# Optimization experiments

Measured on AMD Instinct MI355X. Metric: run time of the kernel, lower is better.

## Reference

```python
import jax, jax.numpy as jnp
import numpy as np

N_GROUPS = 32  # getGroupSize(.) assumed -> channels // 8 (or //24 for 3*ch) == 32 for ch=256
HEADS = 4


def group_norm(x, gamma, beta, groups=N_GROUPS, eps=1e-5):
    n, c = x.shape
    xg = x.reshape(n, groups, c // groups)
    mu = xg.mean(-1, keepdims=True)
    var = xg.var(-1, keepdims=True)
    xn = ((xg - mu) * jax.lax.rsqrt(var + eps)).reshape(n, c)
    return xn * gamma + beta


def setup_inputs():
    key = jax.random.key(0)
    N, E, CH, HID = 2000, 16000, 256, 256
    ks = jax.random.split(key, 24)

    def w(k, shape, s=0.02):
        return (jax.random.normal(k, shape) * s).astype(jnp.float32)

    inp = {
        'x': jax.random.normal(ks[0], (N, CH), jnp.float32),
        'edge_index': jax.random.randint(ks[1], (2, E), 0, N),
        'edge_attr': jax.random.normal(ks[2], (E, CH), jnp.float32),
        # edge_mlp: GN(3ch)+ReLU -> Linear(3ch,hid) -> GN(hid)+ReLU -> Linear(hid,ch)
        'gn_e1_g': jnp.ones((3 * CH,), jnp.float32), 'gn_e1_b': jnp.zeros((3 * CH,), jnp.float32),
        'We1': w(ks[3], (3 * CH, HID)), 'be1': jnp.zeros((HID,), jnp.float32),
        'gn_e2_g': jnp.ones((HID,), jnp.float32), 'gn_e2_b': jnp.zeros((HID,), jnp.float32),
        'We2': w(ks[4], (HID, CH)), 'be2': jnp.zeros((CH,), jnp.float32),
        # actN: GN(ch)+ReLU
        'gn_n_g': jnp.ones((CH,), jnp.float32), 'gn_n_b': jnp.zeros((CH,), jnp.float32),
        # multi-head attention projections
        'Wq': w(ks[5], (CH, CH)), 'bq': jnp.zeros((CH,), jnp.float32),
        'Wk': w(ks[6], (CH, CH)), 'bk': jnp.zeros((CH,), jnp.float32),
        'Wv': w(ks[7], (CH, CH)), 'bv': jnp.zeros((CH,), jnp.float32),
        'Wo': w(ks[8], (CH, CH)), 'bo': jnp.zeros((CH,), jnp.float32),
        # node_mlp: Linear(2ch,hid) -> GN(hid)+ReLU -> Linear(hid,ch)
        'Wn1': w(ks[9], (2 * CH, HID)), 'bn1': jnp.zeros((HID,), jnp.float32),
        'gn_n2_g': jnp.ones((HID,), jnp.float32), 'gn_n2_b': jnp.zeros((HID,), jnp.float32),
        'Wn2': w(ks[10], (HID, CH)), 'bn2': jnp.zeros((CH,), jnp.float32),
    }
    return inp


def reference(x, edge_index, edge_attr,
              gn_e1_g, gn_e1_b, We1, be1, gn_e2_g, gn_e2_b, We2, be2,
              gn_n_g, gn_n_b, Wq, bq, Wk, bk, Wv, bv, Wo, bo,
              Wn1, bn1, gn_n2_g, gn_n2_b, Wn2, bn2):
    row, col = edge_index[0], edge_index[1]
    N, ch = x.shape
    E = edge_attr.shape[0]
    dk = ch // HEADS

    # ---- edge model: cat(src, tgt, e) -> GN/ReLU -> Lin -> GN/ReLU -> Lin (+res) ----
    e_in = jnp.concatenate([x[row], x[col], edge_attr], axis=1)  # [E, 3ch]
    h = jax.nn.relu(group_norm(e_in, gn_e1_g, gn_e1_b))
    h = h @ We1 + be1
    h = jax.nn.relu(group_norm(h, gn_e2_g, gn_e2_b))
    e_out = h @ We2 + be2 + edge_attr  # [E, ch]

    # ---- node model: dense-masked MHA, queries=nodes, keys/values=edges ----
    mask = jnp.zeros((N, E), x.dtype).at[col, jnp.arange(E)].set(1.0)  # scatter adjacency
    q = (x @ Wq + bq).reshape(N, HEADS, dk)
    k = (e_out @ Wk + bk).reshape(E, HEADS, dk)
    v = (e_out @ Wv + bv).reshape(E, HEADS, dk)
    scores = jnp.einsum('nhd,ehd->hne', q, k) / jnp.sqrt(jnp.float32(dk))  # [H, N, E]
    scores = jnp.where(mask[None] > 0, scores, jnp.float32(-1e9))
    attn = jax.nn.softmax(scores, axis=-1)
    g = jnp.einsum('hne,ehd->nhd', attn, v).reshape(N, ch) @ Wo + bo  # [N, ch]

    xa = jax.nn.relu(group_norm(x, gn_n_g, gn_n_b))
    h = jnp.concatenate([xa, g], axis=1) @ Wn1 + bn1  # thinker='cat'
    h = jax.nn.relu(group_norm(h, gn_n2_g, gn_n2_b))
    n_out = h @ Wn2 + bn2 + x  # residual

    return n_out, e_out
```

## Files before the change

kernel.cpp:

```cpp
#include <hip/hip_runtime.h>
#include <hip/hip_bf16.h>
#include <stdint.h>
#include <math.h>

#define CH 256

typedef __attribute__((ext_vector_type(8)))  short short8;
typedef __attribute__((ext_vector_type(16))) short short16;
typedef __attribute__((ext_vector_type(4)))  float f32x4;

#define GL2LDS16(g, l) __builtin_amdgcn_global_load_lds(                       \
    (const __attribute__((address_space(1))) void*)(g),                        \
    (__attribute__((address_space(3))) void*)(l), 16, 0, 0)

__device__ inline short f2bf(float f) {
    __hip_bfloat16 h = __float2bfloat16(f);
    short s;
    __builtin_memcpy(&s, &h, 2);
    return s;
}

__device__ inline float bf2f(short s) {
    unsigned u = ((unsigned)(unsigned short)s) << 16;
    float f;
    __builtin_memcpy(&f, &u, 4);
    return f;
}

__device__ inline float warp_sum64(float v) {
    v += __shfl_xor(v, 32, 64);
    v += __shfl_xor(v, 16, 64);
    v += __shfl_xor(v, 8, 64);
    v += __shfl_xor(v, 4, 64);
    v += __shfl_xor(v, 2, 64);
    v += __shfl_xor(v, 1, 64);
    return v;
}

__device__ inline float warp_max64(float v) {
    v = fmaxf(v, __shfl_xor(v, 32, 64));
    v = fmaxf(v, __shfl_xor(v, 16, 64));
    v = fmaxf(v, __shfl_xor(v, 8, 64));
    v = fmaxf(v, __shfl_xor(v, 4, 64));
    v = fmaxf(v, __shfl_xor(v, 2, 64));
    v = fmaxf(v, __shfl_xor(v, 1, 64));
    return v;
}

struct GArgs {
    const short* A; const short* Bt; const float* bias; const float* res;
    float* C; short* Cbf;
    const float* gamma; const float* beta; float* vbar;
    int M, K, Nc, ldc, coff;
    const short* A2; const short* Bt2; const float* bias2; short* Cbf2;
    int M2, Nc2, y_split;
    const int* coli;
    int* cursor; int* elist;
    const int* counts; int* offsets; int Nn;
};

template <int BM, int BN, int EPI, int DUAL, int VB, int FILL,
          int SCAN = 0, int PAN2 = 0, int XSWZ = 0>
__global__ __launch_bounds__(256) void mfma_gemm(GArgs g)
{
    constexpr int BK = 64;
    constexpr int HM = BM / 2, HN = BN / 2;
    constexpr int FM = HM / 16, FN = HN / 16;
    constexpr int PA = BM / 32;
    constexpr int PB = BN / 32;
    constexpr int NP2 = PAN2 ? 2 : 1;
    __shared__ short As[BM * BK];
    __shared__ short Bs[NP2 * BN * BK];

    const short* A = g.A; const short* Bt = g.Bt;
    const float* bias = g.bias; const float* res = g.res;
    float* C = g.C; short* Cbf = g.Cbf;
    int M = g.M, ldc = g.ldc, co = g.coff;
    const int K = g.K;
    int by = blockIdx.y, bx = blockIdx.x;

    if constexpr (SCAN) {
        if (by == (int)gridDim.y - 1) {
            const int t0 = threadIdx.x;
            if (bx == 0) {
                int* ss = (int*)As;
                int base8 = t0 * 8;
                int loc[8]; int srun = 0;
                #pragma unroll
                for (int j = 0; j < 8; j++) {
                    int idx = base8 + j;
                    int c = (idx < g.Nn) ? g.counts[idx] : 0;
                    loc[j] = srun; srun += c;
                }
                ss[t0] = srun;
                __syncthreads();
                for (int off = 1; off < 256; off <<= 1) {
                    int v = (t0 >= off) ? ss[t0 - off] : 0;
                    __syncthreads();
                    ss[t0] += v;
                    __syncthreads();
                }
                int excl = (t0 > 0) ? ss[t0 - 1] : 0;
                #pragma unroll
                for (int j = 0; j < 8; j++) {
                    int idx = base8 + j;
                    if (idx < g.Nn) {
                        int v = excl + loc[j];
                        g.offsets[idx] = v;
                        g.cursor[idx]  = v;
                    }
                }
                if (t0 == 255) g.offsets[g.Nn] = ss[255];
            }
            return;
        }
    }

    bool qrole = false;
    if constexpr (DUAL) {
        if (by >= g.y_split) {
            by -= g.y_split;
            if (bx * BN >= g.Nc2) return;
            qrole = true;
            A = g.A2; Bt = g.Bt2; bias = g.bias2; Cbf = g.Cbf2;
            C = nullptr; res = nullptr;
            M = g.M2; ldc = g.Nc2; co = 0;
        }
    }

    if constexpr (XSWZ) {
        if (!qrole) {
            int h = by * 4 + bx;
            int lby = (h >> 5) * 8 + (h & 7);
            if (lby * BM >= M) return;
            by = lby;
            bx = (h >> 3) & 3;
        }
    }

    const int t = threadIdx.x;
    const int wave = t >> 6, lane = t & 63;
    const int q = lane >> 4, l16 = lane & 15;
    const int row0 = by * BM;
    const int col0 = bx * BN;
    const int wm = wave & 1, wn = wave >> 1;

    if constexpr (FILL) {
        if (!qrole && bx == 0 && t < BM) {
            int rg = row0 + t;
            if (rg < M) {
                int c = g.coli[rg];
                int p = atomicAdd(&g.cursor[c], 1);
                g.elist[p] = rg;
            }
        }
    }

    f32x4 acc[NP2][FM][FN];
    #pragma unroll
    for (int p2 = 0; p2 < NP2; p2++)
        #pragma unroll
        for (int i = 0; i < FM; i++)
            #pragma unroll
            for (int j = 0; j < FN; j++) acc[p2][i][j] = (f32x4){0.f, 0.f, 0.f, 0.f};

    for (int k0 = 0; k0 < K; k0 += BK) {
        #pragma unroll
        for (int p = 0; p < PA; p++) {
            int chunk = p * 256 + t;
            int r = chunk >> 3;
            int cs = (((chunk & 7) ^ (r & 7)) * 8);
            int gr = row0 + r; if (gr >= M) gr = M - 1;
            const short* gsrc = A + (size_t)gr * K + k0 + cs;
            short* ldst = &As[(p * 256 + wave * 64) * 8];
            GL2LDS16(gsrc, ldst);
        }
        #pragma unroll
        for (int p2 = 0; p2 < NP2; p2++) {
            if (!(PAN2 && p2 == 1 && qrole)) {
                #pragma unroll
                for (int p = 0; p < PB; p++) {
                    int chunk = p * 256 + t;
                    int r = chunk >> 3;
                    int cs = (((chunk & 7) ^ (r & 7)) * 8);
                    const short* gsrc = Bt + (size_t)(col0 + p2 * 256 + r) * K + k0 + cs;
                    short* ldst = &Bs[p2 * BN * BK + (p * 256 + wave * 64) * 8];
                    GL2LDS16(gsrc, ldst);
                }
            }
        }
        __syncthreads();
        #pragma unroll
        for (int ks = 0; ks < 2; ks++) {
            short8 af[FM];
            #pragma unroll
            for (int mi = 0; mi < FM; mi++) {
                int R = wm * HM + mi * 16 + l16;
                int slot = ((ks * 4 + q) ^ (R & 7)) * 8;
                af[mi] = *(const short8*)&As[R * BK + slot];
            }
            #pragma unroll
            for (int p2 = 0; p2 < NP2; p2++) {
                if (!(PAN2 && p2 == 1 && qrole)) {
                    short8 bfr[FN];
                    #pragma unroll
                    for (int ni = 0; ni < FN; ni++) {
                        int R = wn * HN + ni * 16 + l16;
                        int slot = ((ks * 4 + q) ^ (R & 7)) * 8;
                        bfr[ni] = *(const short8*)&Bs[p2 * BN * BK + R * BK + slot];
                    }
                    #pragma unroll
                    for (int mi = 0; mi < FM; mi++)
                        #pragma unroll
                        for (int ni = 0; ni < FN; ni++)
                            acc[p2][mi][ni] = __builtin_amdgcn_mfma_f32_16x16x32_bf16(
                                af[mi], bfr[ni], acc[p2][mi][ni], 0, 0, 0);
                }
            }
        }
        __syncthreads();
    }

    #pragma unroll
    for (int p2 = 0; p2 < NP2; p2++) {
        if (PAN2 && p2 == 1 && qrole) continue;
        #pragma unroll
        for (int ni = 0; ni < FN; ni++) {
            int cg = col0 + p2 * 256 + wn * HN + ni * 16 + l16;
            float bv = bias[cg];
            if constexpr (EPI == 1) {
                float ga = g.gamma[cg], be = g.beta[cg];
                #pragma unroll
                for (int mi = 0; mi < FM; mi++) {
                    #pragma unroll
                    for (int r = 0; r < 4; r++) {
                        float v = acc[p2][mi][ni][r] + bv;
                        float s = v, sq = v * v;
                        s += __shfl_xor(s, 1, 64);  sq += __shfl_xor(sq, 1, 64);
                        s += __shfl_xor(s, 2, 64);  sq += __shfl_xor(sq, 2, 64);
                        s += __shfl_xor(s, 4, 64);  sq += __shfl_xor(sq, 4, 64);
                        float mean = s * 0.125f;
                        float var = sq * 0.125f - mean * mean;
                        float o = fmaxf((v - mean) * rsqrtf(var + 1e-5f) * ga + be, 0.f);
                        int rg = row0 + wm * HM + mi * 16 + q * 4 + r;
                        if (rg < M) Cbf[(size_t)rg * ldc + co + cg] = f2bf(o);
                    }
                }
            } else {
                #pragma unroll
                for (int mi = 0; mi < FM; mi++) {
                    #pragma unroll
                    for (int r = 0; r < 4; r++) {
                        int rg = row0 + wm * HM + mi * 16 + q * 4 + r;
                        if (rg < M) {
                            float v = acc[p2][mi][ni][r] + bv;
                            if (res) v += res[(size_t)rg * ldc + co + cg];
                            if (C)   C[(size_t)rg * ldc + co + cg] = v;
                            if (Cbf) Cbf[(size_t)rg * ldc + co + cg] = f2bf(v);
                        }
                    }
                }
                if constexpr (VB) {
                    bool vpanel = PAN2 ? (p2 == 1) : (!qrole && cg >= 256);
                    if (vpanel) {
                        float part = 0.f;
                        #pragma unroll
                        for (int mi = 0; mi < FM; mi++)
                            #pragma unroll
                            for (int r = 0; r < 4; r++) {
                                int rg = row0 + wm * HM + mi * 16 + q * 4 + r;
                                if (rg < M) part += acc[p2][mi][ni][r] + bv;
                            }
                        part += __shfl_xor(part, 16, 64);
                        part += __shfl_xor(part, 32, 64);
                        if (q == 0) atomicAdd(&g.vbar[cg - 256], part);
                    }
                }
            }
        }
    }
}

struct PrepPack {
    const float* wsrc[8];
    short* wdst[8];
    int wK[8];
    int wstart[8];
    int NW, NP;
    const float* x;
    short* x_bf;
    short* cat_bf;
    float2* xs;
    const float* gng;
    const float* gnb;
    float* vbar;
    const float* bk;
    const float* bv;
    float* bkv;
    int* counts;
    int N;
};

__global__ __launch_bounds__(256) void prep_kernel(PrepPack p)
{
    int bid = blockIdx.x;
    int t = threadIdx.x;
    if (bid < p.NW) {
        int m = 0;
        #pragma unroll
        for (int i = 1; i < 8; i++) if (bid >= p.wstart[i]) m = i;
        int k0 = (bid - p.wstart[m]) * 16;
        const float* src = p.wsrc[m];
        short16 o;
        #pragma unroll
        for (int j = 0; j < 16; j++) o[j] = f2bf(src[(size_t)(k0 + j) * 256 + t]);
        *(short16*)(p.wdst[m] + (size_t)t * p.wK[m] + k0) = o;
        return;
    }
    if (bid >= p.NW + p.NP) {
        int i = (bid - p.NW - p.NP) * 256 + t;
        if (i < p.N) p.counts[i] = 0;
        return;
    }
    int pb = bid - p.NW;
    if (pb == 0) {
        p.vbar[t] = 0.f;
        p.bkv[t] = p.bk[t];
        p.bkv[256 + t] = p.bv[t];
    }
    int r = pb * 8 + (t >> 5);
    int g = t & 31;
    if (r >= p.N) return;
    size_t xb = (size_t)r * CH + g * 8;
    float4 a = *(const float4*)&p.x[xb];
    float4 b = *(const float4*)&p.x[xb + 4];
    short8 xr;
    xr[0] = f2bf(a.x); xr[1] = f2bf(a.y); xr[2] = f2bf(a.z); xr[3] = f2bf(a.w);
    xr[4] = f2bf(b.x); xr[5] = f2bf(b.y); xr[6] = f2bf(b.z); xr[7] = f2bf(b.w);
    *(short8*)&p.x_bf[xb] = xr;
    float s  = a.x + a.y + a.z + a.w + b.x + b.y + b.z + b.w;
    float s2 = a.x*a.x + a.y*a.y + a.z*a.z + a.w*a.w
             + b.x*b.x + b.y*b.y + b.z*b.z + b.w*b.w;
    p.xs[(size_t)r * 32 + g] = make_float2(s, s2);
    float m = s * 0.125f;
    float var = s2 * 0.125f - m * m;
    float rsd = rsqrtf(var + 1e-5f);
    float4 g0 = *(const float4*)&p.gng[g * 8];
    float4 g1 = *(const float4*)&p.gng[g * 8 + 4];
    float4 b0 = *(const float4*)&p.gnb[g * 8];
    float4 b1 = *(const float4*)&p.gnb[g * 8 + 4];
    short8 o;
    o[0] = f2bf(fmaxf((a.x - m) * rsd * g0.x + b0.x, 0.f));
    o[1] = f2bf(fmaxf((a.y - m) * rsd * g0.y + b0.y, 0.f));
    o[2] = f2bf(fmaxf((a.z - m) * rsd * g0.z + b0.z, 0.f));
    o[3] = f2bf(fmaxf((a.w - m) * rsd * g0.w + b0.w, 0.f));
    o[4] = f2bf(fmaxf((b.x - m) * rsd * g1.x + b1.x, 0.f));
    o[5] = f2bf(fmaxf((b.y - m) * rsd * g1.y + b1.y, 0.f));
    o[6] = f2bf(fmaxf((b.z - m) * rsd * g1.z + b1.z, 0.f));
    o[7] = f2bf(fmaxf((b.w - m) * rsd * g1.w + b1.w, 0.f));
    *(short8*)&p.cat_bf[(size_t)r * (2 * CH) + g * 8] = o;
}

__global__ __launch_bounds__(256) void estats_kernel(
    const float* __restrict__ eattr, const int* __restrict__ rowi,
    const int* __restrict__ coli, const float2* __restrict__ xs,
    const short* __restrict__ x_bf,
    const float* __restrict__ g1v, const float* __restrict__ b1v,
    short* __restrict__ e1n, int* __restrict__ counts, int E)
{
    __shared__ float2 ea[8][32];
    __shared__ float2 musr[8][32];
    int t = threadIdx.x;
    int slot = t >> 5, g = t & 31;
    int e = blockIdx.x * 8 + slot;
    float4 a = *(const float4*)&eattr[(size_t)e * CH + g * 8];
    float4 b = *(const float4*)&eattr[(size_t)e * CH + g * 8 + 4];
    float s  = a.x + a.y + a.z + a.w + b.x + b.y + b.z + b.w;
    float s2 = a.x*a.x + a.y*a.y + a.z*a.z + a.w*a.w
             + b.x*b.x + b.y*b.y + b.z*b.z + b.w*b.w;
    ea[slot][g] = make_float2(s, s2);
    int r = rowi[e], c = coli[e];
    if (g == 0) atomicAdd(&counts[c], 1);
    __syncthreads();
    float S = 0.f, S2 = 0.f;
    #pragma unroll
    for (int j = 0; j < 3; j++) {
        int b3 = 3 * g + j;
        int src = b3 >> 5, idx = b3 & 31;
        float2 v;
        if (src == 0)      v = xs[(size_t)r * 32 + idx];
        else if (src == 1) v = xs[(size_t)c * 32 + idx];
        else               v = ea[slot][idx];
        S += v.x; S2 += v.y;
    }
    float m = S * (1.f / 24.f);
    float var = S2 * (1.f / 24.f) - m * m;
    musr[slot][g] = make_float2(m, rsqrtf(var + 1e-5f));
    __syncthreads();
    #pragma unroll
    for (int seg = 0; seg < 3; seg++) {
        int pos = seg * 256 + g * 8;
        float2 ms = musr[slot][pos / 24];
        float4 ga  = *(const float4*)&g1v[pos];
        float4 ga2 = *(const float4*)&g1v[pos + 4];
        float4 gb  = *(const float4*)&b1v[pos];
        float4 gb2 = *(const float4*)&b1v[pos + 4];
        float v0, v1, v2, v3, v4, v5, v6, v7;
        if (seg == 2) {
            v0 = a.x; v1 = a.y; v2 = a.z; v3 = a.w;
            v4 = b.x; v5 = b.y; v6 = b.z; v7 = b.w;
        } else {
            const short* srow = x_bf + (size_t)(seg == 0 ? r : c) * CH + g * 8;
            short8 v8 = *(const short8*)srow;
            v0 = bf2f(v8[0]); v1 = bf2f(v8[1]); v2 = bf2f(v8[2]); v3 = bf2f(v8[3]);
            v4 = bf2f(v8[4]); v5 = bf2f(v8[5]); v6 = bf2f(v8[6]); v7 = bf2f(v8[7]);
        }
        short8 o;
        o[0] = f2bf(fmaxf((v0 - ms.x) * ms.y * ga.x  + gb.x,  0.f));
        o[1] = f2bf(fmaxf((v1 - ms.x) * ms.y * ga.y  + gb.y,  0.f));
        o[2] = f2bf(fmaxf((v2 - ms.x) * ms.y * ga.z  + gb.z,  0.f));
        o[3] = f2bf(fmaxf((v3 - ms.x) * ms.y * ga.w  + gb.w,  0.f));
        o[4] = f2bf(fmaxf((v4 - ms.x) * ms.y * ga2.x + gb2.x, 0.f));
        o[5] = f2bf(fmaxf((v5 - ms.x) * ms.y * ga2.y + gb2.y, 0.f));
        o[6] = f2bf(fmaxf((v6 - ms.x) * ms.y * ga2.z + gb2.z, 0.f));
        o[7] = f2bf(fmaxf((v7 - ms.x) * ms.y * ga2.w + gb2.w, 0.f));
        *(short8*)&e1n[(size_t)e * 768 + pos] = o;
    }
}

__global__ __launch_bounds__(256) void attn_kernel(
    const short* __restrict__ qb, const short* __restrict__ kvb,
    const int* __restrict__ offsets, const int* __restrict__ elist,
    const float* __restrict__ vbar, short* __restrict__ g_bf, int N, int E)
{
    __shared__ int eidx[64];
    __shared__ float scl[4 * 64];
    int n = blockIdx.x;
    int wave = threadIdx.x >> 6;
    int lane = threadIdx.x & 63;
    int s0 = offsets[n], s1 = offsets[n + 1];
    float q0 = bf2f(qb[(size_t)n * CH + lane]);
    float q1 = bf2f(qb[(size_t)n * CH + 64 + lane]);
    float q2 = bf2f(qb[(size_t)n * CH + 128 + lane]);
    float q3 = bf2f(qb[(size_t)n * CH + 192 + lane]);
    float out = 0.f, m = -INFINITY, l = 0.f;
    for (int base = s0; base < s1; base += 64) {
        int cn = s1 - base; if (cn > 64) cn = 64;
        if (wave == 0 && lane < cn) eidx[lane] = elist[base + lane];
        __syncthreads();
        for (int j = wave; j < cn; j += 4) {
            int e = eidx[j];
            const short* kr = kvb + (size_t)e * 512;
            float d0 = warp_sum64(q0 * bf2f(kr[lane]));
            float d1 = warp_sum64(q1 * bf2f(kr[64 + lane]));
            float d2 = warp_sum64(q2 * bf2f(kr[128 + lane]));
            float d3 = warp_sum64(q3 * bf2f(kr[192 + lane]));
            if (lane == 0) {
                scl[j]       = d0 * 0.125f;
                scl[64 + j]  = d1 * 0.125f;
                scl[128 + j] = d2 * 0.125f;
                scl[192 + j] = d3 * 0.125f;
            }
        }
        __syncthreads();
        float s = (lane < cn) ? scl[wave * 64 + lane] : -INFINITY;
        float mc = warp_max64(s);
        float nm = fmaxf(m, mc);
        float scale = __expf(m - nm);
        float pp = (lane < cn) ? __expf(s - nm) : 0.f;
        float ps = warp_sum64(pp);
        l = l * scale + ps;
        out *= scale;
        m = nm;
        for (int i = 0; i < cn; i++) {
            float pi = __shfl(pp, i, 64);
            int ei = eidx[i];
            out += pi * bf2f(kvb[(size_t)ei * 512 + 256 + wave * 64 + lane]);
        }
        __syncthreads();
    }
    float res;
    if (s1 > s0) res = out / l;
    else         res = vbar[wave * 64 + lane] * (1.f / (float)E);
    g_bf[(size_t)n * CH + wave * 64 + lane] = f2bf(res);
}

extern "C" void kernel_launch(void* const* d_in, const int* in_sizes, int n_in,
                              void* d_out, int out_size, void* d_ws, size_t ws_size,
                              hipStream_t stream)
{
    const float* x       = (const float*)d_in[0];
    const int*   ei      = (const int*)d_in[1];
    const float* eattr   = (const float*)d_in[2];
    const float* gn_e1_g = (const float*)d_in[3];
    const float* gn_e1_b = (const float*)d_in[4];
    const float* We1     = (const float*)d_in[5];
    const float* be1     = (const float*)d_in[6];
    const float* gn_e2_g = (const float*)d_in[7];
    const float* gn_e2_b = (const float*)d_in[8];
    const float* We2     = (const float*)d_in[9];
    const float* be2     = (const float*)d_in[10];
    const float* gn_n_g  = (const float*)d_in[11];
    const float* gn_n_b  = (const float*)d_in[12];
    const float* Wq      = (const float*)d_in[13];
    const float* bq      = (const float*)d_in[14];
    const float* Wk      = (const float*)d_in[15];
    const float* bk      = (const float*)d_in[16];
    const float* Wv      = (const float*)d_in[17];
    const float* bv      = (const float*)d_in[18];
    const float* Wo      = (const float*)d_in[19];
    const float* bo      = (const float*)d_in[20];
    const float* Wn1     = (const float*)d_in[21];
    const float* bn1     = (const float*)d_in[22];
    const float* gn_n2_g = (const float*)d_in[23];
    const float* gn_n2_b = (const float*)d_in[24];
    const float* Wn2     = (const float*)d_in[25];
    const float* bn2     = (const float*)d_in[26];

    const int N = in_sizes[0] / CH;
    const int E = in_sizes[2] / CH;

    float* nout = (float*)d_out;
    float* eout = (float*)d_out + (size_t)N * CH;

    char* base = (char*)d_ws;
    short* kv_bf  = (short*)base; base += (size_t)E * 512 * 2;
    short* h2_bf  = (short*)base; base += (size_t)E * CH * 2;
    short* eo_bf  = (short*)base; base += (size_t)E * CH * 2;
    short* e1n    = (short*)base; base += (size_t)E * 768 * 2;
    short* q_bf   = (short*)base; base += (size_t)N * CH * 2;
    short* g_bf   = (short*)base; base += (size_t)N * CH * 2;
    short* cat_bf = (short*)base; base += (size_t)N * 2 * CH * 2;
    short* hn_bf  = (short*)base; base += (size_t)N * CH * 2;
    short* x_bf   = (short*)base; base += (size_t)N * CH * 2;
    float2* xs    = (float2*)base; base += (size_t)N * 32 * 8;
    float* vbar   = (float*)base; base += 1024;
    float* bkv    = (float*)base; base += 2048;
    short* We1t = (short*)base; base += (size_t)768 * 256 * 2;
    short* We2t = (short*)base; base += (size_t)256 * 256 * 2;
    short* Wqt  = (short*)base; base += (size_t)256 * 256 * 2;
    short* Wkvt = (short*)base; base += (size_t)512 * 256 * 2;
    short* Wot  = (short*)base; base += (size_t)256 * 256 * 2;
    short* Wn1t = (short*)base; base += (size_t)512 * 256 * 2;
    short* Wn2t = (short*)base; base += (size_t)256 * 256 * 2;
    int* counts  = (int*)base;
    int* offsets = counts + N;
    int* cursor  = offsets + (N + 1) + 3;
    int* elist   = cursor + N;

    const int* rowi = ei;
    const int* coli = ei + E;

    dim3 blk(256);

    PrepPack pp;
    const float* wsrc[8] = {We1, We2, Wq, Wk, Wv, Wo, Wn1, Wn2};
    short* wdst[8] = {We1t, We2t, Wqt, Wkvt, Wkvt + (size_t)256 * 256, Wot, Wn1t, Wn2t};
    const int wKd[8] = {768, 256, 256, 256, 256, 256, 512, 256};
    int acc = 0;
    for (int i = 0; i < 8; i++) {
        pp.wsrc[i] = wsrc[i]; pp.wdst[i] = wdst[i]; pp.wK[i] = wKd[i];
        pp.wstart[i] = acc; acc += wKd[i] / 16;
    }
    pp.NW = acc;
    pp.NP = (N + 7) / 8;
    pp.x = x; pp.x_bf = x_bf; pp.cat_bf = cat_bf; pp.xs = xs;
    pp.gng = gn_n_g; pp.gnb = gn_n_b;
    pp.vbar = vbar; pp.bk = bk; pp.bv = bv; pp.bkv = bkv;
    pp.counts = counts; pp.N = N;
    int nzero = (N + 255) / 256;
    prep_kernel<<<pp.NW + pp.NP + nzero, blk, 0, stream>>>(pp);

    estats_kernel<<<E / 8, blk, 0, stream>>>(eattr, rowi, coli, xs, x_bf,
                                             gn_e1_g, gn_e1_b, e1n, counts, E);

    GArgs ga = {};
    ga.A = e1n; ga.Bt = We1t; ga.bias = be1; ga.Cbf = h2_bf;
    ga.gamma = gn_e2_g; ga.beta = gn_e2_b;
    ga.M = E; ga.K = 3 * CH; ga.Nc = CH; ga.ldc = CH; ga.coff = 0;
    ga.counts = counts; ga.offsets = offsets; ga.cursor = cursor; ga.Nn = N;
    mfma_gemm<64, 64, 1, 0, 0, 0, 1, 0, 1><<<dim3(4, 257), blk, 0, stream>>>(ga);

    ga = {};
    ga.A = h2_bf; ga.Bt = We2t; ga.bias = be2; ga.res = eattr;
    ga.C = eout; ga.Cbf = eo_bf;
    ga.M = E; ga.K = CH; ga.Nc = CH; ga.ldc = CH; ga.coff = 0;
    mfma_gemm<64, 64, 0, 0, 0, 0, 0, 0, 1><<<dim3(4, 256), blk, 0, stream>>>(ga);

    ga = {};
    ga.A = eo_bf; ga.Bt = Wkvt; ga.bias = bkv; ga.Cbf = kv_bf; ga.vbar = vbar;
    ga.M = E; ga.K = CH; ga.Nc = 512; ga.ldc = 512; ga.coff = 0;
    ga.A2 = x_bf; ga.Bt2 = Wqt; ga.bias2 = bq; ga.Cbf2 = q_bf;
    ga.M2 = N; ga.Nc2 = CH; ga.y_split = 256;
    ga.coli = coli; ga.cursor = cursor; ga.elist = elist;
    mfma_gemm<64, 64, 0, 1, 1, 1, 0, 1, 1><<<dim3(4, 256 + (N + 63) / 64), blk, 0, stream>>>(ga);

    attn_kernel<<<N, blk, 0, stream>>>(q_bf, kv_bf, offsets, elist, vbar, g_bf, N, E);

    ga = {};
    ga.A = g_bf; ga.Bt = Wot; ga.bias = bo; ga.Cbf = cat_bf;
    ga.M = N; ga.K = CH; ga.Nc = CH; ga.ldc = 2 * CH; ga.coff = CH;
    mfma_gemm<32, 64, 0, 0, 0, 0><<<dim3(4, (N + 31) / 32), blk, 0, stream>>>(ga);

    ga = {};
    ga.A = cat_bf; ga.Bt = Wn1t; ga.bias = bn1; ga.Cbf = hn_bf;
    ga.gamma = gn_n2_g; ga.beta = gn_n2_b;
    ga.M = N; ga.K = 2 * CH; ga.Nc = CH; ga.ldc = CH; ga.coff = 0;
    mfma_gemm<32, 64, 1, 0, 0, 0><<<dim3(4, (N + 31) / 32), blk, 0, stream>>>(ga);

    ga = {};
    ga.A = hn_bf; ga.Bt = Wn2t; ga.bias = bn2; ga.res = x; ga.C = nout;
    ga.M = N; ga.K = CH; ga.Nc = CH; ga.ldc = CH; ga.coff = 0;
    mfma_gemm<32, 64, 0, 0, 0, 0><<<dim3(4, (N + 31) / 32), blk, 0, stream>>>(ga);
}
```

Before: 226.4 us.

## Fuse the three node-tail GEMMs into one cooperative kernel with grid syncs

Replaces the three separate node-side GEMM launches (Wo projection, Wn1 with GroupNorm+ReLU, Wn2 with residual) with a single cooperative kernel. The phases are separated by threadfence plus grid-wide sync. This removes two kernel launch gaps and their tail drain. In exchange it adds grid-sync cost and requires all 252 blocks to be co-resident.

```diff
diff --git a/kernel.cpp b/kernel.cpp
--- a/kernel.cpp
+++ b/kernel.cpp
@@ -1,5 +1,6 @@
 #include <hip/hip_runtime.h>
 #include <hip/hip_bf16.h>
+#include <hip/hip_cooperative_groups.h>
 #include <stdint.h>
 #include <math.h>
 
@@ -279,6 +280,122 @@
             }
         }
     }
+}
+
+template <int EPI>
+__device__ __forceinline__ void tail_phase(
+    short* As, short* Bs,
+    const short* A, int K, const short* Bt,
+    const float* bias, const float* res, float* C, short* Cbf,
+    int ldc, int co, const float* gamma, const float* beta, int M)
+{
+    constexpr int BK = 64;
+    const int t = threadIdx.x;
+    const int wave = t >> 6, lane = t & 63;
+    const int q = lane >> 4, l16 = lane & 15;
+    const int by = blockIdx.x >> 2, bx = blockIdx.x & 3;
+    const int row0 = by * 32, col0 = bx * 64;
+    const int wm = wave & 1, wn = wave >> 1;
+
+    f32x4 acc[2];
+    acc[0] = (f32x4){0.f, 0.f, 0.f, 0.f};
+    acc[1] = (f32x4){0.f, 0.f, 0.f, 0.f};
+
+    for (int k0 = 0; k0 < K; k0 += BK) {
+        {
+            int r = t >> 3;
+            int cs = (((t & 7) ^ (r & 7)) * 8);
+            int gr = row0 + r; if (gr >= M) gr = M - 1;
+            GL2LDS16(A + (size_t)gr * K + k0 + cs, &As[(wave * 64) * 8]);
+        }
+        #pragma unroll
+        for (int p = 0; p < 2; p++) {
+            int chunk = p * 256 + t;
+            int r = chunk >> 3;
+            int cs = (((chunk & 7) ^ (r & 7)) * 8);
+            GL2LDS16(Bt + (size_t)(col0 + r) * K + k0 + cs,
+                     &Bs[(p * 256 + wave * 64) * 8]);
+        }
+        __syncthreads();
+        #pragma unroll
+        for (int ks = 0; ks < 2; ks++) {
+            short8 af;
+            {
+                int R = wm * 16 + l16;
+                int slot = ((ks * 4 + q) ^ (R & 7)) * 8;
+                af = *(const short8*)&As[R * BK + slot];
+            }
+            #pragma unroll
+            for (int ni = 0; ni < 2; ni++) {
+                int R = wn * 32 + ni * 16 + l16;
+                int slot = ((ks * 4 + q) ^ (R & 7)) * 8;
+                short8 bf8 = *(const short8*)&Bs[R * BK + slot];
+                acc[ni] = __builtin_amdgcn_mfma_f32_16x16x32_bf16(af, bf8, acc[ni], 0, 0, 0);
+            }
+        }
+        __syncthreads();
+    }
+
+    #pragma unroll
+    for (int ni = 0; ni < 2; ni++) {
+        int cg = col0 + wn * 32 + ni * 16 + l16;
+        float bv = bias[cg];
+        if constexpr (EPI == 1) {
+            float ga = gamma[cg], be = beta[cg];
+            #pragma unroll
+            for (int r = 0; r < 4; r++) {
+                float v = acc[ni][r] + bv;
+                float s = v, sq = v * v;
+                s += __shfl_xor(s, 1, 64);  sq += __shfl_xor(sq, 1, 64);
+                s += __shfl_xor(s, 2, 64);  sq += __shfl_xor(sq, 2, 64);
+                s += __shfl_xor(s, 4, 64);  sq += __shfl_xor(sq, 4, 64);
+                float mean = s * 0.125f;
+                float var = sq * 0.125f - mean * mean;
+                float o = fmaxf((v - mean) * rsqrtf(var + 1e-5f) * ga + be, 0.f);
+                int rg = row0 + wm * 16 + q * 4 + r;
+                if (rg < M) Cbf[(size_t)rg * ldc + co + cg] = f2bf(o);
+            }
+        } else {
+            #pragma unroll
+            for (int r = 0; r < 4; r++) {
+                int rg = row0 + wm * 16 + q * 4 + r;
+                if (rg < M) {
+                    float v = acc[ni][r] + bv;
+                    if (res) v += res[(size_t)rg * ldc + co + cg];
+                    if (C)   C[(size_t)rg * ldc + co + cg] = v;
+                    if (Cbf) Cbf[(size_t)rg * ldc + co + cg] = f2bf(v);
+                }
+            }
+        }
+    }
+}
+
+struct TailCoop {
+    const short* gbf; const short* catbf; const short* hnbf;
+    const short* Wot; const short* Wn1t; const short* Wn2t;
+    const float* bo; const float* bn1; const float* bn2;
+    const float* g2; const float* b2;
+    const float* x; float* nout;
+    short* catw; short* hnw;
+    int M;
+};
+
+__global__ __launch_bounds__(256) void tail_coop(TailCoop a)
+{
+    __shared__ short As[32 * 64];
+    __shared__ short Bs[64 * 64];
+    cooperative_groups::grid_group grid = cooperative_groups::this_grid();
+
+    tail_phase<0>(As, Bs, a.gbf, 256, a.Wot, a.bo,
+                  nullptr, nullptr, a.catw, 512, 256, nullptr, nullptr, a.M);
+    __threadfence();
+    grid.sync();
+    tail_phase<1>(As, Bs, a.catbf, 512, a.Wn1t, a.bn1,
+                  nullptr, nullptr, a.hnw, 256, 0, a.g2, a.b2, a.M);
+    __threadfence();
+    grid.sync();
+    tail_phase<0>(As, Bs, a.hnbf, 256, a.Wn2t, a.bn2,
+                  a.x, a.nout, nullptr, 256, 0, nullptr, nullptr, a.M);
 }
 
 struct PrepPack {
@@ -597,19 +714,15 @@
 
     attn_kernel<<<N, blk, 0, stream>>>(q_bf, kv_bf, offsets, elist, vbar, g_bf, N, E);
 
-    ga = {};
-    ga.A = g_bf; ga.Bt = Wot; ga.bias = bo; ga.Cbf = cat_bf;
-    ga.M = N; ga.K = CH; ga.Nc = CH; ga.ldc = 2 * CH; ga.coff = CH;
-    mfma_gemm<32, 64, 0, 0, 0, 0><<<dim3(4, (N + 31) / 32), blk, 0, stream>>>(ga);
-
-    ga = {};
-    ga.A = cat_bf; ga.Bt = Wn1t; ga.bias = bn1; ga.Cbf = hn_bf;
-    ga.gamma = gn_n2_g; ga.beta = gn_n2_b;
-    ga.M = N; ga.K = 2 * CH; ga.Nc = CH; ga.ldc = CH; ga.coff = 0;
-    mfma_gemm<32, 64, 1, 0, 0, 0><<<dim3(4, (N + 31) / 32), blk, 0, stream>>>(ga);
-
-    ga = {};
-    ga.A = hn_bf; ga.Bt = Wn2t; ga.bias = bn2; ga.res = x; ga.C = nout;
-    ga.M = N; ga.K = CH; ga.Nc = CH; ga.ldc = CH; ga.coff = 0;
-    mfma_gemm<32, 64, 0, 0, 0, 0><<<dim3(4, (N + 31) / 32), blk, 0, stream>>>(ga);
-}
+    TailCoop tc;
+    tc.gbf = g_bf; tc.catbf = cat_bf; tc.hnbf = hn_bf;
+    tc.Wot = Wot; tc.Wn1t = Wn1t; tc.Wn2t = Wn2t;
+    tc.bo = bo; tc.bn1 = bn1; tc.bn2 = bn2;
+    tc.g2 = gn_n2_g; tc.b2 = gn_n2_b;
+    tc.x = x; tc.nout = nout;
+    tc.catw = cat_bf; tc.hnw = hn_bf;
+    tc.M = N;
+    void* kargs[] = { &tc };
+    hipLaunchCooperativeKernel((void*)tail_coop, dim3(4 * ((N + 31) / 32)),
+                               dim3(256), kargs, 0, stream);
+}
```

Measured after the change: 366.1 us. +61.7%, slower.

## Fold Wo projection into Wn1 and drop the output-projection GEMM

Applied to the files above, without the earlier changes.

Precomputes Wo·Wn1[256:] and the combined bias bn1 + bo·Wn1[256:] in the prep kernel, so the attention output goes straight into the second half of the concatenated buffer. The separate Wo GEMM launch and its intermediate g_bf round trip are removed. In exchange, 256 extra prep blocks each do a 256x256 fp32 dot-product column, and the fused weight is rounded to bf16 once, which slightly changes numerics.

```diff
diff --git a/kernel.cpp b/kernel.cpp
--- a/kernel.cpp
+++ b/kernel.cpp
@@ -282,11 +282,14 @@
 }
 
 struct PrepPack {
-    const float* wsrc[8];
-    short* wdst[8];
-    int wK[8];
-    int wstart[8];
-    int NW, NP;
+    const float* wsrc[7];
+    short* wdst[7];
+    int wK[7];
+    int wE[7];
+    int wstart[7];
+    int NW, NF, NP;
+    const float* Wo; const float* Wn1s; const float* bo; const float* bn1;
+    short* Wn1t; float* b2f;
     const float* x;
     short* x_bf;
     short* cat_bf;
@@ -308,7 +311,7 @@
     if (bid < p.NW) {
         int m = 0;
         #pragma unroll
-        for (int i = 1; i < 8; i++) if (bid >= p.wstart[i]) m = i;
+        for (int i = 1; i < 7; i++) if (bid >= p.wstart[i]) m = i;
         int k0 = (bid - p.wstart[m]) * 16;
         const float* src = p.wsrc[m];
         short16 o;
@@ -317,12 +320,30 @@
         *(short16*)(p.wdst[m] + (size_t)t * p.wK[m] + k0) = o;
         return;
     }
-    if (bid >= p.NW + p.NP) {
-        int i = (bid - p.NW - p.NP) * 256 + t;
+    if (bid < p.NW + p.NF) {
+        int c = bid - p.NW;
+        __shared__ float colv[256];
+        __shared__ float red[4];
+        colv[t] = p.Wn1s[(size_t)(256 + t) * 256 + c];
+        __syncthreads();
+        const float* wrow = p.Wo + (size_t)t * 256;
+        float acc = 0.f;
+        #pragma unroll 4
+        for (int j = 0; j < 256; j++) acc += wrow[j] * colv[j];
+        p.Wn1t[(size_t)c * 512 + 256 + t] = f2bf(acc);
+        float bvp = p.bo[t] * colv[t];
+        bvp = warp_sum64(bvp);
+        if ((t & 63) == 0) red[t >> 6] = bvp;
+        __syncthreads();
+        if (t == 0) p.b2f[c] = p.bn1[c] + red[0] + red[1] + red[2] + red[3];
+        return;
+    }
+    if (bid >= p.NW + p.NF + p.NP) {
+        int i = (bid - p.NW - p.NF - p.NP) * 256 + t;
         if (i < p.N) p.counts[i] = 0;
         return;
     }
-    int pb = bid - p.NW;
+    int pb = bid - p.NW - p.NF;
     if (pb == 0) {
         p.vbar[t] = 0.f;
         p.bkv[t] = p.bk[t];
@@ -431,7 +452,7 @@
 __global__ __launch_bounds__(256) void attn_kernel(
     const short* __restrict__ qb, const short* __restrict__ kvb,
     const int* __restrict__ offsets, const int* __restrict__ elist,
-    const float* __restrict__ vbar, short* __restrict__ g_bf, int N, int E)
+    const float* __restrict__ vbar, short* __restrict__ gout, int N, int E)
 {
     __shared__ int eidx[64];
     __shared__ float scl[4 * 64];
@@ -482,7 +503,7 @@
     float res;
     if (s1 > s0) res = out / l;
     else         res = vbar[wave * 64 + lane] * (1.f / (float)E);
-    g_bf[(size_t)n * CH + wave * 64 + lane] = f2bf(res);
+    gout[(size_t)n * 512 + wave * 64 + lane] = f2bf(res);
 }
 
 extern "C" void kernel_launch(void* const* d_in, const int* in_sizes, int n_in,
@@ -536,11 +557,11 @@
     float2* xs    = (float2*)base; base += (size_t)N * 32 * 8;
     float* vbar   = (float*)base; base += 1024;
     float* bkv    = (float*)base; base += 2048;
+    float* b2f    = (float*)base; base += 1024;
     short* We1t = (short*)base; base += (size_t)768 * 256 * 2;
     short* We2t = (short*)base; base += (size_t)256 * 256 * 2;
     short* Wqt  = (short*)base; base += (size_t)256 * 256 * 2;
     short* Wkvt = (short*)base; base += (size_t)512 * 256 * 2;
-    short* Wot  = (short*)base; base += (size_t)256 * 256 * 2;
     short* Wn1t = (short*)base; base += (size_t)512 * 256 * 2;
     short* Wn2t = (short*)base; base += (size_t)256 * 256 * 2;
     int* counts  = (int*)base;
@@ -550,26 +571,32 @@
 
     const int* rowi = ei;
     const int* coli = ei + E;
+    (void)g_bf;
 
     dim3 blk(256);
 
     PrepPack pp;
-    const float* wsrc[8] = {We1, We2, Wq, Wk, Wv, Wo, Wn1, Wn2};
-    short* wdst[8] = {We1t, We2t, Wqt, Wkvt, Wkvt + (size_t)256 * 256, Wot, Wn1t, Wn2t};
-    const int wKd[8] = {768, 256, 256, 256, 256, 256, 512, 256};
+    const float* wsrc[7] = {We1, We2, Wq, Wk, Wv, Wn1, Wn2};
+    short* wdst[7] = {We1t, We2t, Wqt, Wkvt, Wkvt + (size_t)256 * 256, Wn1t, Wn2t};
+    const int wKd[7] = {768, 256, 256, 256, 256, 512, 256};
+    const int wEd[7] = {768, 256, 256, 256, 256, 256, 256};
     int acc = 0;
-    for (int i = 0; i < 8; i++) {
-        pp.wsrc[i] = wsrc[i]; pp.wdst[i] = wdst[i]; pp.wK[i] = wKd[i];
-        pp.wstart[i] = acc; acc += wKd[i] / 16;
+    for (int i = 0; i < 7; i++) {
+        pp.wsrc[i] = wsrc[i]; pp.wdst[i] = wdst[i];
+        pp.wK[i] = wKd[i]; pp.wE[i] = wEd[i];
+        pp.wstart[i] = acc; acc += wEd[i] / 16;
     }
     pp.NW = acc;
+    pp.NF = 256;
     pp.NP = (N + 7) / 8;
+    pp.Wo = Wo; pp.Wn1s = Wn1; pp.bo = bo; pp.bn1 = bn1;
+    pp.Wn1t = Wn1t; pp.b2f = b2f;
     pp.x = x; pp.x_bf = x_bf; pp.cat_bf = cat_bf; pp.xs = xs;
     pp.gng = gn_n_g; pp.gnb = gn_n_b;
     pp.vbar = vbar; pp.bk = bk; pp.bv = bv; pp.bkv = bkv;
     pp.counts = counts; pp.N = N;
     int nzero = (N + 255) / 256;
-    prep_kernel<<<pp.NW + pp.NP + nzero, blk, 0, stream>>>(pp);
+    prep_kernel<<<pp.NW + pp.NF + pp.NP + nzero, blk, 0, stream>>>(pp);
 
     estats_kernel<<<E / 8, blk, 0, stream>>>(eattr, rowi, coli, xs, x_bf,
                                              gn_e1_g, gn_e1_b, e1n, counts, E);
@@ -595,15 +622,11 @@
     ga.coli = coli; ga.cursor = cursor; ga.elist = elist;
     mfma_gemm<64, 64, 0, 1, 1, 1, 0, 1, 1><<<dim3(4, 256 + (N + 63) / 64), blk, 0, stream>>>(ga);
 
-    attn_kernel<<<N, blk, 0, stream>>>(q_bf, kv_bf, offsets, elist, vbar, g_bf, N, E);
+    attn_kernel<<<N, blk, 0, stream>>>(q_bf, kv_bf, offsets, elist, vbar,
+                                       cat_bf + 256, N, E);
 
     ga = {};
-    ga.A = g_bf; ga.Bt = Wot; ga.bias = bo; ga.Cbf = cat_bf;
-    ga.M = N; ga.K = CH; ga.Nc = CH; ga.ldc = 2 * CH; ga.coff = CH;
-    mfma_gemm<32, 64, 0, 0, 0, 0><<<dim3(4, (N + 31) / 32), blk, 0, stream>>>(ga);
-
-    ga = {};
-    ga.A = cat_bf; ga.Bt = Wn1t; ga.bias = bn1; ga.Cbf = hn_bf;
+    ga.A = cat_bf; ga.Bt = Wn1t; ga.bias = b2f; ga.Cbf = hn_bf;
     ga.gamma = gn_n2_g; ga.beta = gn_n2_b;
     ga.M = N; ga.K = 2 * CH; ga.Nc = CH; ga.ldc = CH; ga.coff = 0;
     mfma_gemm<32, 64, 1, 0, 0, 0><<<dim3(4, (N + 31) / 32), blk, 0, stream>>>(ga);
```

Result: no change. 230.5 us (+1.8%).
